# Optimization experiments

Hardware: AMD Instinct MI355X
Metric: run time of the kernel (lower is better)

The kernel has to match this reference:

```python
import jax, jax.numpy as jnp
import numpy as np

N, IN_DIM, OUT_DIM, E = 50000, 64, 64, 800000


def setup_inputs() -> dict:
    key = jax.random.key(0)
    k1, k2, k3, k4 = jax.random.split(key, 4)
    x = jax.random.normal(k1, (N, IN_DIM), dtype=jnp.float32)
    edge_index = jax.random.randint(k2, (2, E), 0, N, dtype=jnp.int64)
    # nn.Linear(in_dim, out_dim): weight [out, in], bias [out]
    bound = 1.0 / np.sqrt(IN_DIM)
    W = jax.random.uniform(k3, (OUT_DIM, IN_DIM), minval=-bound, maxval=bound, dtype=jnp.float32)
    b = jax.random.uniform(k4, (OUT_DIM,), minval=-bound, maxval=bound, dtype=jnp.float32)
    return {"x": x, "edge_index": edge_index, "W": W, "b": b}


def reference(x, edge_index, W, b):
    row, col = edge_index[0], edge_index[1]
    n = x.shape[0]
    # deg = bincount(row, minlength=N) + 1e-6, shape [N, 1]
    deg = jnp.zeros((n,), dtype=jnp.float32).at[row].add(1.0)[:, None] + 1e-6
    # agg[row] += x[col]  (gather + scatter-add)
    agg = jnp.zeros_like(x).at[row].add(x[col])
    agg = agg / deg
    return agg @ W.T + b
```

## Files before the change

### kernel.cpp

```cpp
#include <hip/hip_runtime.h>
#include <hip/hip_bf16.h>

#define N_NODES 50000
#define DIM 64
#define N_EDGES 800000
#define CAP 64
#define NTHR 256
#define GB_ROWS 32
#define SLICE 6250
#define NGROUP 196
#define TOTAL_BLOCKS (NGROUP * 24)
#define CHUNK_EDGES 2048


typedef __attribute__((ext_vector_type(8))) short bf16x8;
typedef __attribute__((ext_vector_type(4))) float f32x4;

static __device__ inline unsigned int f2bf(float f) {
    __hip_bfloat16 h = __float2bfloat16(f);
    return (unsigned int)*reinterpret_cast<unsigned short*>(&h);
}
static __device__ inline float bf_lo(unsigned int u) { return __uint_as_float(u << 16); }
static __device__ inline float bf_hi(unsigned int u) { return __uint_as_float(u & 0xffff0000u); }

__global__ __launch_bounds__(NTHR, 8) void place_gemm_kernel(
    const int* __restrict__ ei, const float* __restrict__ x,
    const float* __restrict__ W, int* __restrict__ count,
    int* csr, unsigned short* __restrict__ yb)
{
    __shared__ float4 xs4[GB_ROWS * 16];
    __shared__ uint4  Wb[512];

    int t = threadIdx.x;
    int b = blockIdx.x;
    int m = b % 24;

    if (m < 8) {
        int g  = (b / 24) * 8 + m;
        int R0 = g * GB_ROWS;
        if (R0 < N_NODES) {
            const float4* x4 = (const float4*)x;
            for (int i = t; i < GB_ROWS * 16; i += NTHR) {
                int r = i >> 4, c = i & 15;
                int q = (R0 + r) * 16 + c;
                float4 v = (q < N_NODES * 16) ? x4[q]
                                              : make_float4(0.f, 0.f, 0.f, 0.f);
                xs4[(r << 4) | (c ^ (r & 15))] = v;
            }
            for (int i = t; i < 512; i += NTHR) {
                int n = i >> 3, kg = i & 7;
                const float* wr = W + n * DIM + kg * 8;
                uint4 uw;
                uw.x = f2bf(wr[0]) | (f2bf(wr[1]) << 16);
                uw.y = f2bf(wr[2]) | (f2bf(wr[3]) << 16);
                uw.z = f2bf(wr[4]) | (f2bf(wr[5]) << 16);
                uw.w = f2bf(wr[6]) | (f2bf(wr[7]) << 16);
                Wb[(n << 3) | (kg ^ (n & 7))] = uw;
            }
            __syncthreads();

            int w  = t >> 6, l = t & 63;
            int rt = w >> 1, ch = w & 1;
            int lm = l & 15, lg = l >> 4;
            int mloc = rt * 16 + lm;

            f32x4 acc0 = {0.f, 0.f, 0.f, 0.f};
            f32x4 acc1 = {0.f, 0.f, 0.f, 0.f};
#pragma unroll
            for (int kc = 0; kc < 2; kc++) {
                int c0 = kc * 8 + lg * 2;
                float4 xa = xs4[(mloc << 4) | ((c0    ) ^ lm)];
                float4 xb = xs4[(mloc << 4) | ((c0 + 1) ^ lm)];
                float xv[8] = {xa.x, xa.y, xa.z, xa.w, xb.x, xb.y, xb.z, xb.w};
                bf16x8 ahi, alo;
#pragma unroll
                for (int j = 0; j < 8; j++) {
                    unsigned hb = f2bf(xv[j]);
                    float lo = xv[j] - __uint_as_float(hb << 16);
                    ahi[j] = (short)hb;
                    alo[j] = (short)f2bf(lo);
                }
                int kgg = kc * 4 + lg;
#pragma unroll
                for (int ctl = 0; ctl < 2; ctl++) {
                    int n = (ch * 2 + ctl) * 16 + lm;
                    uint4 wq = Wb[(n << 3) | (kgg ^ (n & 7))];
                    bf16x8 bfr = *reinterpret_cast<bf16x8*>(&wq);
                    if (ctl == 0) {
                        acc0 = __builtin_amdgcn_mfma_f32_16x16x32_bf16(ahi, bfr, acc0, 0, 0, 0);
                        acc0 = __builtin_amdgcn_mfma_f32_16x16x32_bf16(alo, bfr, acc0, 0, 0, 0);
                    } else {
                        acc1 = __builtin_amdgcn_mfma_f32_16x16x32_bf16(ahi, bfr, acc1, 0, 0, 0);
                        acc1 = __builtin_amdgcn_mfma_f32_16x16x32_bf16(alo, bfr, acc1, 0, 0, 0);
                    }
                }
            }
#pragma unroll
            for (int ctl = 0; ctl < 2; ctl++) {
                f32x4 acc = ctl ? acc1 : acc0;
                int n = (ch * 2 + ctl) * 16 + lm;
#pragma unroll
                for (int q = 0; q < 4; q++) {
                    int rr = R0 + rt * 16 + lg * 4 + q;
                    if (rr < N_NODES)
                        yb[(size_t)rr * DIM + n] = (unsigned short)f2bf(acc[q]);
                }
            }
        }
    } else {
        int s    = b & 7;
        int lo   = s * SLICE;
        int q    = (b / 24) * 2 + ((m - 8) >> 3);
        int e0   = q * CHUNK_EDGES + t * 8;
        if (e0 < N_EDGES) {
            const int4* rp = (const int4*)(ei + e0);
            int4 ra = rp[0];
            int4 rb = rp[1];
            int rows[8] = {ra.x, ra.y, ra.z, ra.w, rb.x, rb.y, rb.z, rb.w};
#pragma unroll
            for (int k = 0; k < 8; k++) {
                if ((unsigned)(rows[k] - lo) < (unsigned)SLICE) {
                    int col = ei[N_EDGES + e0 + k];
                    int pos = atomicAdd(&count[rows[k]], 1);
                    if (pos < CAP) csr[rows[k] * CAP + pos] = col;
                }
            }
        }
    }
}

__global__ __launch_bounds__(NTHR) void agg_kernel(
    const unsigned short* __restrict__ yb, const int* __restrict__ count,
    const int* csr, const float* __restrict__ bias, float* out)
{
    int t   = threadIdx.x;
    int w   = t >> 6;
    int l   = t & 63;
    int sub = l & 7;
    int grp = l >> 3;
    int sb  = blockIdx.x & 7;
    int i   = blockIdx.x >> 3;
    int rl  = i * 4 + w;
    if (rl >= SLICE) return;
    int r = sb * SLICE + rl;

    int deg = count[r];
    int dc  = deg < CAP ? deg : CAP;
    int myc = csr[(size_t)r * CAP + l];

    const uint4* ybq = (const uint4*)yb;
    float s[8];
#pragma unroll
    for (int q = 0; q < 8; q++) s[q] = 0.f;

    bool valid = grp < dc;
    {
        int c0 = __shfl(myc, grp);
        int cs = valid ? c0 : 0;
        uint4 v = ybq[(size_t)cs * 8 + sub];
        for (int jb = 8; jb < dc; jb += 8) {
            int  j2     = jb + grp;
            int  c2     = __shfl(myc, j2);
            bool valid2 = j2 < dc;
            int  cs2    = valid2 ? c2 : 0;
            uint4 v2 = ybq[(size_t)cs2 * 8 + sub];
            if (valid) {
                s[0] += bf_lo(v.x); s[1] += bf_hi(v.x);
                s[2] += bf_lo(v.y); s[3] += bf_hi(v.y);
                s[4] += bf_lo(v.z); s[5] += bf_hi(v.z);
                s[6] += bf_lo(v.w); s[7] += bf_hi(v.w);
            }
            v = v2; valid = valid2;
        }
        if (valid) {
            s[0] += bf_lo(v.x); s[1] += bf_hi(v.x);
            s[2] += bf_lo(v.y); s[3] += bf_hi(v.y);
            s[4] += bf_lo(v.z); s[5] += bf_hi(v.z);
            s[6] += bf_lo(v.w); s[7] += bf_hi(v.w);
        }
    }
#pragma unroll
    for (int q = 0; q < 8; q++) {
        s[q] += __shfl_xor(s[q], 8);
        s[q] += __shfl_xor(s[q], 16);
        s[q] += __shfl_xor(s[q], 32);
    }

    if (grp == 0) {
        float inv_d = 1.0f / ((float)deg + 1e-6f);
        float4 b0 = ((const float4*)bias)[2 * sub];
        float4 b1 = ((const float4*)bias)[2 * sub + 1];
        float4 o0 = make_float4(s[0] * inv_d + b0.x, s[1] * inv_d + b0.y,
                                s[2] * inv_d + b0.z, s[3] * inv_d + b0.w);
        float4 o1 = make_float4(s[4] * inv_d + b1.x, s[5] * inv_d + b1.y,
                                s[6] * inv_d + b1.z, s[7] * inv_d + b1.w);
        ((float4*)(out + (size_t)r * DIM))[2 * sub]     = o0;
        ((float4*)(out + (size_t)r * DIM))[2 * sub + 1] = o1;
    }
}

extern "C" void kernel_launch(void* const* d_in, const int* in_sizes, int n_in,
                              void* d_out, int out_size, void* d_ws, size_t ws_size,
                              hipStream_t stream) {
    const float* x    = (const float*)d_in[0];
    const int*   ei   = (const int*)d_in[1];
    const float* W    = (const float*)d_in[2];
    const float* bias = (const float*)d_in[3];
    float* out = (float*)d_out;

    int*            count = (int*)d_ws;
    unsigned short* yb    = (unsigned short*)((char*)d_ws + 262144);
    int*            csr   = (int*)d_out;

    hipMemsetAsync(count, 0, N_NODES * sizeof(int), stream);
    place_gemm_kernel<<<TOTAL_BLOCKS, NTHR, 0, stream>>>(ei, x, W, count, csr, yb);
    agg_kernel<<<8 * 1563, NTHR, 0, stream>>>(yb, count, csr, bias, out);
}
```

Measured before the change: 128.7 us.

## Fuse memset, place/GEMM and aggregation into one cooperative persistent kernel

Replaces the memset plus two kernel launches with one cooperative kernel. It zeroes the counts, runs the place and GEMM units, then runs the aggregation units, with grid-wide syncs between the phases. Blocks loop over the work units persistently, with the grid sized from an occupancy query. The aim is to remove launch gaps and the separate memset, at the cost of two grid.sync barriers and possibly lower occupancy per phase. The old three-launch path is kept as a fallback if the cooperative launch fails.

```diff
diff --git a/kernel.cpp b/kernel.cpp
--- a/kernel.cpp
+++ b/kernel.cpp
@@ -1,5 +1,8 @@
 #include <hip/hip_runtime.h>
 #include <hip/hip_bf16.h>
+#include <hip/hip_cooperative_groups.h>
+
+namespace cg = cooperative_groups;
 
 #define N_NODES 50000
 #define DIM 64
@@ -9,7 +12,8 @@
 #define GB_ROWS 32
 #define SLICE 6250
 #define NGROUP 196
-#define TOTAL_BLOCKS (NGROUP * 24)
+#define TOTAL_UNITS (NGROUP * 24)
+#define AGG_UNITS (8 * 1563)
 #define CHUNK_EDGES 2048
 
 
@@ -23,123 +27,122 @@
 static __device__ inline float bf_lo(unsigned int u) { return __uint_as_float(u << 16); }
 static __device__ inline float bf_hi(unsigned int u) { return __uint_as_float(u & 0xffff0000u); }
 
-__global__ __launch_bounds__(NTHR, 8) void place_gemm_kernel(
-    const int* __restrict__ ei, const float* __restrict__ x,
-    const float* __restrict__ W, int* __restrict__ count,
-    int* csr, unsigned short* __restrict__ yb)
-{
-    __shared__ float4 xs4[GB_ROWS * 16];
-    __shared__ uint4  Wb[512];
-
-    int t = threadIdx.x;
-    int b = blockIdx.x;
-    int m = b % 24;
-
-    if (m < 8) {
-        int g  = (b / 24) * 8 + m;
-        int R0 = g * GB_ROWS;
-        if (R0 < N_NODES) {
-            const float4* x4 = (const float4*)x;
-            for (int i = t; i < GB_ROWS * 16; i += NTHR) {
-                int r = i >> 4, c = i & 15;
-                int q = (R0 + r) * 16 + c;
-                float4 v = (q < N_NODES * 16) ? x4[q]
-                                              : make_float4(0.f, 0.f, 0.f, 0.f);
-                xs4[(r << 4) | (c ^ (r & 15))] = v;
+static __device__ inline void gemm_unit(int u, int t, float4* xs4, uint4* Wb,
+                                        const float* __restrict__ x,
+                                        const float* __restrict__ W,
+                                        unsigned short* __restrict__ yb)
+{
+    int g  = (u / 24) * 8 + (u % 24);
+    int R0 = g * GB_ROWS;
+    if (R0 >= N_NODES) return;
+
+    const float4* x4 = (const float4*)x;
+    for (int i = t; i < GB_ROWS * 16; i += NTHR) {
+        int r = i >> 4, c = i & 15;
+        int q = (R0 + r) * 16 + c;
+        float4 v = (q < N_NODES * 16) ? x4[q] : make_float4(0.f, 0.f, 0.f, 0.f);
+        xs4[(r << 4) | (c ^ (r & 15))] = v;
+    }
+    for (int i = t; i < 512; i += NTHR) {
+        int n = i >> 3, kg = i & 7;
+        const float* wr = W + n * DIM + kg * 8;
+        uint4 uw;
+        uw.x = f2bf(wr[0]) | (f2bf(wr[1]) << 16);
+        uw.y = f2bf(wr[2]) | (f2bf(wr[3]) << 16);
+        uw.z = f2bf(wr[4]) | (f2bf(wr[5]) << 16);
+        uw.w = f2bf(wr[6]) | (f2bf(wr[7]) << 16);
+        Wb[(n << 3) | (kg ^ (n & 7))] = uw;
+    }
+    __syncthreads();
+
+    int w  = t >> 6, l = t & 63;
+    int rt = w >> 1, ch = w & 1;
+    int lm = l & 15, lg = l >> 4;
+    int mloc = rt * 16 + lm;
+
+    f32x4 acc0 = {0.f, 0.f, 0.f, 0.f};
+    f32x4 acc1 = {0.f, 0.f, 0.f, 0.f};
+#pragma unroll
+    for (int kc = 0; kc < 2; kc++) {
+        int c0 = kc * 8 + lg * 2;
+        float4 xa = xs4[(mloc << 4) | ((c0    ) ^ lm)];
+        float4 xb = xs4[(mloc << 4) | ((c0 + 1) ^ lm)];
+        float xv[8] = {xa.x, xa.y, xa.z, xa.w, xb.x, xb.y, xb.z, xb.w};
+        bf16x8 ahi, alo;
+#pragma unroll
+        for (int j = 0; j < 8; j++) {
+            unsigned hb = f2bf(xv[j]);
+            float lo = xv[j] - __uint_as_float(hb << 16);
+            ahi[j] = (short)hb;
+            alo[j] = (short)f2bf(lo);
+        }
+        int kgg = kc * 4 + lg;
+#pragma unroll
+        for (int ctl = 0; ctl < 2; ctl++) {
+            int n = (ch * 2 + ctl) * 16 + lm;
+            uint4 wq = Wb[(n << 3) | (kgg ^ (n & 7))];
+            bf16x8 bfr = *reinterpret_cast<bf16x8*>(&wq);
+            if (ctl == 0) {
+                acc0 = __builtin_amdgcn_mfma_f32_16x16x32_bf16(ahi, bfr, acc0, 0, 0, 0);
+                acc0 = __builtin_amdgcn_mfma_f32_16x16x32_bf16(alo, bfr, acc0, 0, 0, 0);
+            } else {
+                acc1 = __builtin_amdgcn_mfma_f32_16x16x32_bf16(ahi, bfr, acc1, 0, 0, 0);
+                acc1 = __builtin_amdgcn_mfma_f32_16x16x32_bf16(alo, bfr, acc1, 0, 0, 0);
             }
-            for (int i = t; i < 512; i += NTHR) {
-                int n = i >> 3, kg = i & 7;
-                const float* wr = W + n * DIM + kg * 8;
-                uint4 uw;
-                uw.x = f2bf(wr[0]) | (f2bf(wr[1]) << 16);
-                uw.y = f2bf(wr[2]) | (f2bf(wr[3]) << 16);
-                uw.z = f2bf(wr[4]) | (f2bf(wr[5]) << 16);
-                uw.w = f2bf(wr[6]) | (f2bf(wr[7]) << 16);
-                Wb[(n << 3) | (kg ^ (n & 7))] = uw;
+        }
+    }
+#pragma unroll
+    for (int ctl = 0; ctl < 2; ctl++) {
+        f32x4 acc = ctl ? acc1 : acc0;
+        int n = (ch * 2 + ctl) * 16 + lm;
+#pragma unroll
+        for (int q = 0; q < 4; q++) {
+            int rr = R0 + rt * 16 + lg * 4 + q;
+            if (rr < N_NODES)
+                yb[(size_t)rr * DIM + n] = (unsigned short)f2bf(acc[q]);
+        }
+    }
+    __syncthreads();
+}
+
+static __device__ inline void place_unit(int u, int t,
+                                         const int* __restrict__ ei,
+                                         int* __restrict__ count, int* csr)
+{
+    int m    = u % 24;
+    int s    = u & 7;
+    int lo   = s * SLICE;
+    int q    = (u / 24) * 2 + ((m - 8) >> 3);
+    int e0   = q * CHUNK_EDGES + t * 8;
+    if (e0 < N_EDGES) {
+        const int4* rp = (const int4*)(ei + e0);
+        int4 ra = rp[0];
+        int4 rb = rp[1];
+        int rows[8] = {ra.x, ra.y, ra.z, ra.w, rb.x, rb.y, rb.z, rb.w};
+#pragma unroll
+        for (int k = 0; k < 8; k++) {
+            if ((unsigned)(rows[k] - lo) < (unsigned)SLICE) {
+                int col = ei[N_EDGES + e0 + k];
+                int pos = atomicAdd(&count[rows[k]], 1);
+                if (pos < CAP) csr[rows[k] * CAP + pos] = col;
             }
-            __syncthreads();
-
-            int w  = t >> 6, l = t & 63;
-            int rt = w >> 1, ch = w & 1;
-            int lm = l & 15, lg = l >> 4;
-            int mloc = rt * 16 + lm;
-
-            f32x4 acc0 = {0.f, 0.f, 0.f, 0.f};
-            f32x4 acc1 = {0.f, 0.f, 0.f, 0.f};
-#pragma unroll
-            for (int kc = 0; kc < 2; kc++) {
-                int c0 = kc * 8 + lg * 2;
-                float4 xa = xs4[(mloc << 4) | ((c0    ) ^ lm)];
-                float4 xb = xs4[(mloc << 4) | ((c0 + 1) ^ lm)];
-                float xv[8] = {xa.x, xa.y, xa.z, xa.w, xb.x, xb.y, xb.z, xb.w};
-                bf16x8 ahi, alo;
-#pragma unroll
-                for (int j = 0; j < 8; j++) {
-                    unsigned hb = f2bf(xv[j]);
-                    float lo = xv[j] - __uint_as_float(hb << 16);
-                    ahi[j] = (short)hb;
-                    alo[j] = (short)f2bf(lo);
-                }
-                int kgg = kc * 4 + lg;
-#pragma unroll
-                for (int ctl = 0; ctl < 2; ctl++) {
-                    int n = (ch * 2 + ctl) * 16 + lm;
-                    uint4 wq = Wb[(n << 3) | (kgg ^ (n & 7))];
-                    bf16x8 bfr = *reinterpret_cast<bf16x8*>(&wq);
-                    if (ctl == 0) {
-                        acc0 = __builtin_amdgcn_mfma_f32_16x16x32_bf16(ahi, bfr, acc0, 0, 0, 0);
-                        acc0 = __builtin_amdgcn_mfma_f32_16x16x32_bf16(alo, bfr, acc0, 0, 0, 0);
-                    } else {
-                        acc1 = __builtin_amdgcn_mfma_f32_16x16x32_bf16(ahi, bfr, acc1, 0, 0, 0);
-                        acc1 = __builtin_amdgcn_mfma_f32_16x16x32_bf16(alo, bfr, acc1, 0, 0, 0);
-                    }
-                }
-            }
-#pragma unroll
-            for (int ctl = 0; ctl < 2; ctl++) {
-                f32x4 acc = ctl ? acc1 : acc0;
-                int n = (ch * 2 + ctl) * 16 + lm;
-#pragma unroll
-                for (int q = 0; q < 4; q++) {
-                    int rr = R0 + rt * 16 + lg * 4 + q;
-                    if (rr < N_NODES)
-                        yb[(size_t)rr * DIM + n] = (unsigned short)f2bf(acc[q]);
-                }
-            }
-        }
-    } else {
-        int s    = b & 7;
-        int lo   = s * SLICE;
-        int q    = (b / 24) * 2 + ((m - 8) >> 3);
-        int e0   = q * CHUNK_EDGES + t * 8;
-        if (e0 < N_EDGES) {
-            const int4* rp = (const int4*)(ei + e0);
-            int4 ra = rp[0];
-            int4 rb = rp[1];
-            int rows[8] = {ra.x, ra.y, ra.z, ra.w, rb.x, rb.y, rb.z, rb.w};
-#pragma unroll
-            for (int k = 0; k < 8; k++) {
-                if ((unsigned)(rows[k] - lo) < (unsigned)SLICE) {
-                    int col = ei[N_EDGES + e0 + k];
-                    int pos = atomicAdd(&count[rows[k]], 1);
-                    if (pos < CAP) csr[rows[k] * CAP + pos] = col;
-                }
-            }
-        }
-    }
-}
-
-__global__ __launch_bounds__(NTHR) void agg_kernel(
-    const unsigned short* __restrict__ yb, const int* __restrict__ count,
-    const int* csr, const float* __restrict__ bias, float* out)
-{
-    int t   = threadIdx.x;
+        }
+    }
+}
+
+static __device__ inline void agg_unit(int u, int t,
+                                       const unsigned short* __restrict__ yb,
+                                       const int* __restrict__ count,
+                                       const int* csr,
+                                       const float* __restrict__ bias,
+                                       float* out)
+{
     int w   = t >> 6;
     int l   = t & 63;
     int sub = l & 7;
     int grp = l >> 3;
-    int sb  = blockIdx.x & 7;
-    int i   = blockIdx.x >> 3;
+    int sb  = u & 7;
+    int i   = u >> 3;
     int rl  = i * 4 + w;
     if (rl >= SLICE) return;
     int r = sb * SLICE + rl;
@@ -199,6 +202,50 @@
     }
 }
 
+__global__ __launch_bounds__(NTHR, 4) void fused_kernel(
+    const int* __restrict__ ei, const float* __restrict__ x,
+    const float* __restrict__ W, const float* __restrict__ bias,
+    int* count, int* csr, unsigned short* yb, float* out)
+{
+    cg::grid_group grid = cg::this_grid();
+    __shared__ float4 xs4[GB_ROWS * 16];
+    __shared__ uint4  Wb[512];
+
+    int t = threadIdx.x, bid = blockIdx.x, B = gridDim.x;
+
+    for (int i = bid * NTHR + t; i < N_NODES; i += B * NTHR)
+        count[i] = 0;
+    grid.sync();
+
+    for (int u = bid; u < TOTAL_UNITS; u += B) {
+        if (u % 24 < 8) gemm_unit(u, t, xs4, Wb, x, W, yb);
+        else            place_unit(u, t, ei, count, csr);
+    }
+    grid.sync();
+
+    for (int u = bid; u < AGG_UNITS; u += B)
+        agg_unit(u, t, yb, count, csr, bias, out);
+}
+
+__global__ __launch_bounds__(NTHR, 8) void place_gemm_kernel(
+    const int* __restrict__ ei, const float* __restrict__ x,
+    const float* __restrict__ W, int* __restrict__ count,
+    int* csr, unsigned short* __restrict__ yb)
+{
+    __shared__ float4 xs4[GB_ROWS * 16];
+    __shared__ uint4  Wb[512];
+    int u = blockIdx.x, t = threadIdx.x;
+    if (u % 24 < 8) gemm_unit(u, t, xs4, Wb, x, W, yb);
+    else            place_unit(u, t, ei, count, csr);
+}
+
+__global__ __launch_bounds__(NTHR) void agg_kernel(
+    const unsigned short* __restrict__ yb, const int* __restrict__ count,
+    const int* csr, const float* __restrict__ bias, float* out)
+{
+    agg_unit(blockIdx.x, threadIdx.x, yb, count, csr, bias, out);
+}
+
 extern "C" void kernel_launch(void* const* d_in, const int* in_sizes, int n_in,
                               void* d_out, int out_size, void* d_ws, size_t ws_size,
                               hipStream_t stream) {
@@ -212,7 +259,29 @@
     unsigned short* yb    = (unsigned short*)((char*)d_ws + 262144);
     int*            csr   = (int*)d_out;
 
-    hipMemsetAsync(count, 0, N_NODES * sizeof(int), stream);
-    place_gemm_kernel<<<TOTAL_BLOCKS, NTHR, 0, stream>>>(ei, x, W, count, csr, yb);
-    agg_kernel<<<8 * 1563, NTHR, 0, stream>>>(yb, count, csr, bias, out);
-}
+    static int nblk = 0;
+    if (nblk == 0) {
+        int per_cu = 0;
+        if (hipOccupancyMaxActiveBlocksPerMultiprocessor(
+                &per_cu, fused_kernel, NTHR, 0) != hipSuccess || per_cu < 1)
+            per_cu = 0;
+        if (per_cu > 8) per_cu = 8;
+        nblk = per_cu * 256;
+        if (nblk > 2048) nblk = 2048;
+        if (nblk == 0) nblk = -1;
+    }
+
+    bool coop_ok = (nblk > 0);
+    if (coop_ok) {
+        void* args[] = {(void*)&ei, (void*)&x, (void*)&W, (void*)&bias,
+                        (void*)&count, (void*)&csr, (void*)&yb, (void*)&out};
+        hipError_t e = hipLaunchCooperativeKernel(fused_kernel, dim3(nblk),
+                                                  dim3(NTHR), args, 0, stream);
+        if (e != hipSuccess) coop_ok = false;
+    }
+    if (!coop_ok) {
+        hipMemsetAsync(count, 0, N_NODES * sizeof(int), stream);
+        place_gemm_kernel<<<TOTAL_UNITS, NTHR, 0, stream>>>(ei, x, W, count, csr, yb);
+        agg_kernel<<<AGG_UNITS, NTHR, 0, stream>>>(yb, count, csr, bias, out);
+    }
+}
```

Result: slower. 450.2 us (+249.8%).
